# Kernel tuning notes

Measured on AMD Instinct MI355X. Metric: run time of the kernel, lower is better.

The kernel has to match this reference:

```python
import jax, jax.numpy as jnp
import numpy as np

N = 50000   # nodes per graph
E = 800000  # edges per graph (even, message() splits in half)
F = 100     # node/edge feature dim (init_count_size / init_emb_size)
D = 64      # hidden_dim3 = rule_graph_dim
W_SCALE = 0.05


def _mlp(x, w1, b1, w2, b2):
    return jax.nn.relu(x @ w1 + b1) @ w2 + b2


def _triple_conv(x, src, dst, ea, lw, lb, l2w, l2b, nn_fn):
    # PyG flow source_to_target: x_j = x[edge_index[0]], x_i = x[edge_index[1]]
    h = ea.shape[0] // 2
    x_j = x[src]
    x_i = x[dst]
    m1 = jax.nn.relu(jnp.concatenate([x_i[:h], ea[:h], x_j[:h]], 1) @ lw + lb)
    m2 = jax.nn.relu(jnp.concatenate([x_j[h:], ea[h:], x_i[h:]], 1) @ l2w + l2b)
    msgs = jnp.concatenate([m1, m2], 0)
    agg = jax.ops.segment_sum(msgs, dst, num_segments=x.shape[0])
    # eps = 0.0 buffer -> out = agg + (1+eps)*x = agg + x
    return nn_fn(agg + x)


def setup_inputs() -> dict:
    key = jax.random.key(0)
    ks = jax.random.split(key, 32)
    inp = {
        'features_1': jax.random.normal(ks[0], (N, F), jnp.float32),
        'edge_index_1': jax.random.randint(ks[1], (2, E), 0, N, jnp.int64 if jax.config.jax_enable_x64 else jnp.int32).astype(jnp.int32),
        'edge_attr_1': jax.random.normal(ks[2], (E, F), jnp.float32),
        'features_2': jax.random.normal(ks[3], (N, F), jnp.float32),
        'edge_index_2': jax.random.randint(ks[4], (2, E), 0, N, jnp.int32),
        'edge_attr_2': jax.random.normal(ks[5], (E, F), jnp.float32),
        'c1_lin_w': jax.random.normal(ks[6], (3 * F, F), jnp.float32) * W_SCALE,
        'c1_lin_b': jax.random.normal(ks[7], (F,), jnp.float32) * W_SCALE,
        'c1_lin2_w': jax.random.normal(ks[8], (3 * F, F), jnp.float32) * W_SCALE,
        'c1_lin2_b': jax.random.normal(ks[9], (F,), jnp.float32) * W_SCALE,
        'mlp1_w1': jax.random.normal(ks[10], (F, F), jnp.float32) * W_SCALE,
        'mlp1_b1': jax.random.normal(ks[11], (F,), jnp.float32) * W_SCALE,
        'mlp1_w2': jax.random.normal(ks[12], (F, F), jnp.float32) * W_SCALE,
        'mlp1_b2': jax.random.normal(ks[13], (F,), jnp.float32) * W_SCALE,
        'c2_lin_w': jax.random.normal(ks[14], (3 * F, F), jnp.float32) * W_SCALE,
        'c2_lin_b': jax.random.normal(ks[15], (F,), jnp.float32) * W_SCALE,
        'c2_lin2_w': jax.random.normal(ks[16], (3 * F, F), jnp.float32) * W_SCALE,
        'c2_lin2_b': jax.random.normal(ks[17], (F,), jnp.float32) * W_SCALE,
        'mlp2_w1': jax.random.normal(ks[18], (F, D), jnp.float32) * W_SCALE,
        'mlp2_b1': jax.random.normal(ks[19], (D,), jnp.float32) * W_SCALE,
        'mlp2_w2': jax.random.normal(ks[20], (D, D), jnp.float32) * W_SCALE,
        'mlp2_b2': jax.random.normal(ks[21], (D,), jnp.float32) * W_SCALE,
    }
    return inp


def reference(features_1, edge_index_1, edge_attr_1,
              features_2, edge_index_2, edge_attr_2,
              c1_lin_w, c1_lin_b, c1_lin2_w, c1_lin2_b,
              mlp1_w1, mlp1_b1, mlp1_w2, mlp1_b2,
              c2_lin_w, c2_lin_b, c2_lin2_w, c2_lin2_b,
              mlp2_w1, mlp2_b1, mlp2_w2, mlp2_b2):

    def conv_pass(x, ei, ea):
        src, dst = ei[0], ei[1]
        x = _triple_conv(x, src, dst, ea, c1_lin_w, c1_lin_b, c1_lin2_w, c1_lin2_b,
                         lambda z: _mlp(z, mlp1_w1, mlp1_b1, mlp1_w2, mlp1_b2))
        x = jax.nn.relu(x)
        x = _triple_conv(x, src, dst, ea, c2_lin_w, c2_lin_b, c2_lin2_w, c2_lin2_b,
                         lambda z: _mlp(z, mlp2_w1, mlp2_b1, mlp2_w2, mlp2_b2))
        return x

    f1 = conv_pass(features_1, edge_index_1, edge_attr_1)  # [N, D]
    f2 = conv_pass(features_2, edge_index_2, edge_attr_2)  # [N, D]
    # global_add_pool with a single batch id -> sum over nodes
    g1 = jnp.sum(f1, axis=0)
    g2 = jnp.sum(f2, axis=0)
    return jnp.stack([g1, g2], 0)  # [2, D]
```

## Files before the change

kernel.cpp:

```cpp
#include <hip/hip_runtime.h>

#define F 100
#define TS 256

typedef __attribute__((ext_vector_type(4))) unsigned short us4;
typedef __attribute__((ext_vector_type(8))) short short8;
typedef __attribute__((ext_vector_type(4))) float f32x4;

static __device__ __forceinline__ unsigned short f2bf(float f) {
    unsigned int u = __float_as_uint(f);
    unsigned int r = (u + 0x7FFF + ((u >> 16) & 1)) >> 16;
    return (unsigned short)r;
}
static __device__ __forceinline__ float bf2f(unsigned short u) {
    return __uint_as_float(((unsigned int)u) << 16);
}

__global__ __launch_bounds__(TS)
void hist2_kernel(const int* __restrict__ dst0, const int* __restrict__ dst1,
                  int h, int E, int N,
                  int* __restrict__ cnt1, int* __restrict__ cnt2)
{
    for (int idx = blockIdx.x * TS + threadIdx.x; idx < 2 * E; idx += gridDim.x * TS) {
        int g = idx >= E;
        int e = idx - g * E;
        int d = (g ? dst1 : dst0)[e];
        atomicAdd((e < h ? cnt1 : cnt2) + g * N + d, 1);
    }
}

__global__ __launch_bounds__(1024)
void scan4_kernel(const int* __restrict__ cnt1, const int* __restrict__ cnt2,
                  int* __restrict__ rp1, int* __restrict__ rp2, int n)
{
    const int which = blockIdx.x;
    const int hf = which >> 1, g = which & 1;
    const int* cnt = (hf ? cnt2 : cnt1) + g * n;
    int* rp = (hf ? rp2 : rp1) + g * (n + 1);
    __shared__ int buf[1024];
    __shared__ int carry_s;
    const int t = threadIdx.x;
    if (t == 0) carry_s = 0;
    __syncthreads();
    for (int base = 0; base < n; base += 8192) {
        int v[8], s = 0;
        #pragma unroll
        for (int j = 0; j < 8; ++j) {
            int idx = base + t * 8 + j;
            int x = (idx < n) ? cnt[idx] : 0;
            v[j] = s; s += x;
        }
        buf[t] = s;
        __syncthreads();
        for (int off = 1; off < 1024; off <<= 1) {
            int y = (t >= off) ? buf[t - off] : 0;
            __syncthreads();
            buf[t] += y;
            __syncthreads();
        }
        int excl = carry_s + buf[t] - s;
        #pragma unroll
        for (int j = 0; j < 8; ++j) {
            int idx = base + t * 8 + j;
            if (idx < n) rp[idx] = excl + v[j];
        }
        __syncthreads();
        if (t == 1023) carry_s += buf[1023];
        __syncthreads();
    }
    if (t == 0) rp[n] = carry_s;
}

__global__ __launch_bounds__(TS)
void scatter2_kernel(const int* __restrict__ src0, const int* __restrict__ dst0,
                     const int* __restrict__ src1, const int* __restrict__ dst1,
                     int h, int E, int N,
                     const int* __restrict__ rp1, const int* __restrict__ rp2,
                     int* __restrict__ cur1, int* __restrict__ cur2,
                     int* __restrict__ perm1, int* __restrict__ perm2,
                     int* __restrict__ es1, int* __restrict__ es2)
{
    for (int idx = blockIdx.x * TS + threadIdx.x; idx < 2 * E; idx += gridDim.x * TS) {
        int g = idx >= E;
        int e = idx - g * E;
        int d = (g ? dst1 : dst0)[e];
        int s = (g ? src1 : src0)[e];
        if (e < h) {
            int p = rp1[g * (N + 1) + d] + atomicAdd(&cur1[g * N + d], 1);
            perm1[g * h + p] = e; es1[g * h + p] = s + g * N;
        } else {
            int p = rp2[g * (N + 1) + d] + atomicAdd(&cur2[g * N + d], 1);
            perm2[g * h + p] = e; es2[g * h + p] = s + g * N;
        }
    }
}

__global__ __launch_bounds__(TS)
void pack_w_kernel(const float* w0, const float* w1, const float* w2, const float* w3,
                   unsigned short* __restrict__ Wp)
{
    int i = blockIdx.x * TS + threadIdx.x;
    if (i >= 12 * 112 * 128) return;
    int s = i / (112 * 128);
    int r = i - s * (112 * 128);
    int c = r >> 7, k = r & 127;
    int wi = s & 3, grp = s >> 2;
    const float* w = (wi == 0) ? w0 : (wi == 1) ? w1 : (wi == 2) ? w2 : w3;
    int off = (grp == 0) ? F : ((grp == 1) ? 0 : 2 * F);
    unsigned short v = 0;
    if (c < 100 && k < 100) v = f2bf(w[(off + k) * F + c]);
    Wp[i] = v;
}

__global__ __launch_bounds__(TS)
void pack_w2_kernel(const float* __restrict__ w, int K, int Nc, int ldb,
                    unsigned short* __restrict__ out)
{
    int i = blockIdx.x * TS + threadIdx.x;
    if (i >= 112 * 128) return;
    int c = i >> 7, k = i & 127;
    unsigned short v = 0;
    if (c < Nc && k < K) v = f2bf(w[k * ldb + c]);
    out[i] = v;
}

__global__ __launch_bounds__(TS)
void pack_x2_kernel(const float* __restrict__ x0, const float* __restrict__ x1,
                    int N, unsigned short* __restrict__ xb)
{
    const size_t total = (size_t)N * 2 * 32;
    for (size_t i = (size_t)blockIdx.x * TS + threadIdx.x; i < total; i += (size_t)gridDim.x * TS) {
        int n = (int)(i >> 5), q = (int)(i & 31);
        int g = n >= N;
        const float* x = g ? x1 : x0;
        int nl = n - g * N;
        us4 o = (us4){0, 0, 0, 0};
        if (q < 25) {
            float4 v = *(const float4*)&x[(size_t)nl * 100 + q * 4];
            o.x = f2bf(v.x); o.y = f2bf(v.y); o.z = f2bf(v.z); o.w = f2bf(v.w);
        }
        *(us4*)&xb[((size_t)n << 7) + q * 4] = o;
    }
}

__global__ __launch_bounds__(TS)
void gemm_node_mfma(const unsigned short* __restrict__ xb,
                    const unsigned short* __restrict__ B0, const unsigned short* __restrict__ B1,
                    const unsigned short* __restrict__ B2, const unsigned short* __restrict__ B3,
                    unsigned short* __restrict__ NTb,
                    int M)
{
    const int t = threadIdx.x, lane = t & 63, wv = t >> 6;
    const int rA = lane & 15, kg = lane >> 4;
    const unsigned short* Bp[4] = {B0, B1, B2, B3};
    const int ntiles = (M + 15) >> 4;
    for (int tile = blockIdx.x * 4 + wv; tile < ntiles; tile += gridDim.x * 4) {
        const int base = tile << 4;
        const int arow = min(base + rA, M - 1);
        short8 A[4];
        #pragma unroll
        for (int ks = 0; ks < 4; ++ks)
            A[ks] = *(const short8*)&xb[((size_t)arow << 7) + ks * 32 + kg * 8];
        const int row = base + rA;
        #pragma unroll
        for (int sel = 0; sel < 4; ++sel) {
            const unsigned short* B = Bp[sel];
            f32x4 C[7];
            #pragma unroll
            for (int nf = 0; nf < 7; ++nf) C[nf] = (f32x4){0.f, 0.f, 0.f, 0.f};
            #pragma unroll
            for (int ks = 0; ks < 4; ++ks) {
                #pragma unroll
                for (int nf = 0; nf < 7; ++nf) {
                    short8 Bf = *(const short8*)&B[(size_t)(rA + nf * 16) * 128 + ks * 32 + kg * 8];
                    C[nf] = __builtin_amdgcn_mfma_f32_16x16x32_bf16(Bf, A[ks], C[nf], 0, 0, 0);
                }
            }
            if (row < M) {
                #pragma unroll
                for (int nf = 0; nf < 7; ++nf) {
                    const int cb = nf * 16 + kg * 4;
                    if (cb < 100) {
                        us4 o;
                        o.x = f2bf(C[nf][0]); o.y = f2bf(C[nf][1]);
                        o.z = f2bf(C[nf][2]); o.w = f2bf(C[nf][3]);
                        *(us4*)&NTb[(size_t)row * 400 + sel * 100 + cb] = o;
                    }
                }
            }
        }
    }
}

__global__ __launch_bounds__(TS)
void gemm_edge_quad(const float* __restrict__ ea0, const float* __restrict__ ea1,
                    const int* __restrict__ perm,
                    const unsigned short* __restrict__ W0,
                    const unsigned short* __restrict__ W1,
                    unsigned short* __restrict__ P0,
                    unsigned short* __restrict__ P1,
                    int h)
{
    __shared__ unsigned short sA[2][64][136];
    const int t = threadIdx.x, lane = t & 63, wv = t >> 6;
    const int rA = lane & 15, kg = lane >> 4;
    const int M = 2 * h;
    const int ngrp = M >> 6;
    const int r_loc = t >> 2, sub = t & 3;

    int grp = blockIdx.x;
    if (grp >= ngrp) return;

    {
        const int grow = (grp << 6) + r_loc;
        const int g = grow >= h;
        const int e = perm[grow];
        const float* ea = (g ? ea1 : ea0) + (size_t)e * 100;
        float4 raw[7];
        #pragma unroll
        for (int j = 0; j < 7; ++j) {
            const int q = sub + 4 * j;
            if (q < 25) raw[j] = *(const float4*)&ea[q * 4];
        }
        #pragma unroll
        for (int j = 0; j < 8; ++j) {
            const int q = sub + 4 * j;
            us4 o = (us4){0, 0, 0, 0};
            if (j < 7 && q < 25) {
                o.x = f2bf(raw[j].x); o.y = f2bf(raw[j].y);
                o.z = f2bf(raw[j].z); o.w = f2bf(raw[j].w);
            }
            if (q < 32) *(us4*)&sA[0][r_loc][q * 4] = o;
        }
    }
    __syncthreads();

    int cur = 0;
    while (true) {
        const int nxt = grp + gridDim.x;
        const bool more = nxt < ngrp;

        float4 raw[7];
        if (more) {
            const int grow = (nxt << 6) + r_loc;
            const int g = grow >= h;
            const int e = perm[grow];
            const float* ea = (g ? ea1 : ea0) + (size_t)e * 100;
            #pragma unroll
            for (int j = 0; j < 7; ++j) {
                const int q = sub + 4 * j;
                if (q < 25) raw[j] = *(const float4*)&ea[q * 4];
            }
        }

        {
            const int lrow = wv * 16 + rA;
            short8 A[4];
            #pragma unroll
            for (int ks = 0; ks < 4; ++ks)
                A[ks] = *(const short8*)&sA[cur][lrow][ks * 32 + kg * 8];

            f32x4 C0[7], C1[7];
            #pragma unroll
            for (int nf = 0; nf < 7; ++nf) {
                C0[nf] = (f32x4){0.f, 0.f, 0.f, 0.f};
                C1[nf] = (f32x4){0.f, 0.f, 0.f, 0.f};
            }
            #pragma unroll
            for (int ks = 0; ks < 4; ++ks) {
                #pragma unroll
                for (int nf = 0; nf < 7; ++nf) {
                    short8 B0f = *(const short8*)&W0[(size_t)(rA + nf * 16) * 128 + ks * 32 + kg * 8];
                    C0[nf] = __builtin_amdgcn_mfma_f32_16x16x32_bf16(B0f, A[ks], C0[nf], 0, 0, 0);
                    short8 B1f = *(const short8*)&W1[(size_t)(rA + nf * 16) * 128 + ks * 32 + kg * 8];
                    C1[nf] = __builtin_amdgcn_mfma_f32_16x16x32_bf16(B1f, A[ks], C1[nf], 0, 0, 0);
                }
            }
            const int row = (grp << 6) + lrow;
            #pragma unroll
            for (int nf = 0; nf < 7; ++nf) {
                const int cb = nf * 16 + kg * 4;
                if (cb < 100) {
                    us4 o0, o1;
                    o0.x = f2bf(C0[nf][0]); o0.y = f2bf(C0[nf][1]);
                    o0.z = f2bf(C0[nf][2]); o0.w = f2bf(C0[nf][3]);
                    o1.x = f2bf(C1[nf][0]); o1.y = f2bf(C1[nf][1]);
                    o1.z = f2bf(C1[nf][2]); o1.w = f2bf(C1[nf][3]);
                    *(us4*)&P0[(size_t)row * 100 + cb] = o0;
                    *(us4*)&P1[(size_t)row * 100 + cb] = o1;
                }
            }
        }

        if (!more) break;

        #pragma unroll
        for (int j = 0; j < 8; ++j) {
            const int q = sub + 4 * j;
            us4 o = (us4){0, 0, 0, 0};
            if (j < 7 && q < 25) {
                o.x = f2bf(raw[j].x); o.y = f2bf(raw[j].y);
                o.z = f2bf(raw[j].z); o.w = f2bf(raw[j].w);
            }
            if (q < 32) *(us4*)&sA[cur ^ 1][r_loc][q * 4] = o;
        }
        __syncthreads();
        cur ^= 1; grp = nxt;
    }
}

__global__ __launch_bounds__(TS)
void seg_reduce_fused(const unsigned short* __restrict__ PA,
                      const unsigned short* __restrict__ PB,
                      const int* __restrict__ es1, const int* __restrict__ es2,
                      const int* __restrict__ rp1, const int* __restrict__ rp2,
                      const float* __restrict__ cb, const float* __restrict__ cb2,
                      const unsigned short* __restrict__ NTb,
                      const float* __restrict__ x0, const float* __restrict__ x1,
                      const unsigned short* __restrict__ xbin,
                      unsigned short* __restrict__ Ab,
                      int N, int h, int mode)
{
    const int gid = blockIdx.x * TS + threadIdx.x;
    const int n = gid >> 5, q = gid & 31;
    if (n >= 2 * N) return;
    const int c4 = q * 4;
    if (q >= 25) {
        *(us4*)&Ab[((size_t)n << 7) + c4] = (us4){0, 0, 0, 0};
        return;
    }
    const int g = n >= N;
    const int nl = n - g * N;

    float d1x, d1y, d1z, d1w, d2x, d2y, d2z, d2w;
    {
        const us4 vd1 = *(const us4*)&NTb[(size_t)n * 400 + 0 * 100 + c4];
        const float4 b1 = *(const float4*)&cb[c4];
        d1x = bf2f(vd1.x) + b1.x; d1y = bf2f(vd1.y) + b1.y;
        d1z = bf2f(vd1.z) + b1.z; d1w = bf2f(vd1.w) + b1.w;
        const us4 vd2 = *(const us4*)&NTb[(size_t)n * 400 + 3 * 100 + c4];
        const float4 b2 = *(const float4*)&cb2[c4];
        d2x = bf2f(vd2.x) + b2.x; d2y = bf2f(vd2.y) + b2.y;
        d2z = bf2f(vd2.z) + b2.z; d2w = bf2f(vd2.w) + b2.w;
    }
    const int* rpg1 = rp1 + g * (N + 1);
    const int* rpg2 = rp2 + g * (N + 1);
    int pos1 = max(rpg1[nl], 0) + g * h;
    const int end1 = min(rpg1[nl + 1], h) + g * h;
    int pos2 = max(rpg2[nl], 0) + g * h;
    const int end2 = min(rpg2[nl + 1], h) + g * h;

    float ax = 0.f, ay = 0.f, az = 0.f, aw = 0.f;

    const int common = min(end1 - pos1, end2 - pos2);
    #pragma unroll 2
    for (int i = 0; i < common; ++i) {
        const int s1 = es1[pos1 + i];
        const int s2 = es2[pos2 + i];
        const us4 pv1 = *(const us4*)&PA[(size_t)(pos1 + i) * 100 + c4];
        const us4 pv2 = *(const us4*)&PB[(size_t)(pos2 + i) * 100 + c4];
        const us4 v1 = *(const us4*)&NTb[(size_t)s1 * 400 + 1 * 100 + c4];
        const us4 v2 = *(const us4*)&NTb[(size_t)s2 * 400 + 2 * 100 + c4];
        ax += fmaxf(bf2f(pv1.x) + bf2f(v1.x) + d1x, 0.f)
            + fmaxf(bf2f(pv2.x) + bf2f(v2.x) + d2x, 0.f);
        ay += fmaxf(bf2f(pv1.y) + bf2f(v1.y) + d1y, 0.f)
            + fmaxf(bf2f(pv2.y) + bf2f(v2.y) + d2y, 0.f);
        az += fmaxf(bf2f(pv1.z) + bf2f(v1.z) + d1z, 0.f)
            + fmaxf(bf2f(pv2.z) + bf2f(v2.z) + d2z, 0.f);
        aw += fmaxf(bf2f(pv1.w) + bf2f(v1.w) + d1w, 0.f)
            + fmaxf(bf2f(pv2.w) + bf2f(v2.w) + d2w, 0.f);
    }
    pos1 += common; pos2 += common;

    #pragma unroll 2
    for (; pos1 < end1; ++pos1) {
        const int s = es1[pos1];
        const us4 pv = *(const us4*)&PA[(size_t)pos1 * 100 + c4];
        const us4 vs = *(const us4*)&NTb[(size_t)s * 400 + 1 * 100 + c4];
        ax += fmaxf(bf2f(pv.x) + bf2f(vs.x) + d1x, 0.f);
        ay += fmaxf(bf2f(pv.y) + bf2f(vs.y) + d1y, 0.f);
        az += fmaxf(bf2f(pv.z) + bf2f(vs.z) + d1z, 0.f);
        aw += fmaxf(bf2f(pv.w) + bf2f(vs.w) + d1w, 0.f);
    }
    #pragma unroll 2
    for (; pos2 < end2; ++pos2) {
        const int s = es2[pos2];
        const us4 pv = *(const us4*)&PB[(size_t)pos2 * 100 + c4];
        const us4 vs = *(const us4*)&NTb[(size_t)s * 400 + 2 * 100 + c4];
        ax += fmaxf(bf2f(pv.x) + bf2f(vs.x) + d2x, 0.f);
        ay += fmaxf(bf2f(pv.y) + bf2f(vs.y) + d2y, 0.f);
        az += fmaxf(bf2f(pv.z) + bf2f(vs.z) + d2z, 0.f);
        aw += fmaxf(bf2f(pv.w) + bf2f(vs.w) + d2w, 0.f);
    }

    float4 xv;
    if (mode == 0) {
        const float* x = g ? x1 : x0;
        xv = *(const float4*)&x[(size_t)nl * 100 + c4];
    } else {
        const us4 v = *(const us4*)&xbin[((size_t)n << 7) + c4];
        xv.x = bf2f(v.x); xv.y = bf2f(v.y); xv.z = bf2f(v.z); xv.w = bf2f(v.w);
    }
    us4 o;
    o.x = f2bf(ax + xv.x); o.y = f2bf(ay + xv.y);
    o.z = f2bf(az + xv.z); o.w = f2bf(aw + xv.w);
    *(us4*)&Ab[((size_t)n << 7) + c4] = o;
}

__global__ __launch_bounds__(TS)
void gemm_mlp_bf16out(const unsigned short* __restrict__ Ab,
                      const unsigned short* __restrict__ Wp,
                      const float* __restrict__ bias,
                      unsigned short* __restrict__ out,
                      int M, int Nc)
{
    const int t = threadIdx.x, lane = t & 63, wv = t >> 6;
    const int rA = lane & 15, kg = lane >> 4;
    const int ntiles = (M + 15) >> 4;
    for (int tile = blockIdx.x * 4 + wv; tile < ntiles; tile += gridDim.x * 4) {
        const int base = tile << 4;
        const int arow = min(base + rA, M - 1);
        f32x4 C[7];
        #pragma unroll
        for (int nf = 0; nf < 7; ++nf) C[nf] = (f32x4){0.f, 0.f, 0.f, 0.f};
        #pragma unroll
        for (int ks = 0; ks < 4; ++ks) {
            short8 A = *(const short8*)&Ab[((size_t)arow << 7) + ks * 32 + kg * 8];
            #pragma unroll
            for (int nf = 0; nf < 7; ++nf) {
                short8 B = *(const short8*)&Wp[(size_t)(rA + nf * 16) * 128 + ks * 32 + kg * 8];
                C[nf] = __builtin_amdgcn_mfma_f32_16x16x32_bf16(B, A, C[nf], 0, 0, 0);
            }
        }
        const int row = base + rA;
        if (row < M) {
            #pragma unroll
            for (int nf = 0; nf < 7; ++nf) {
                const int cb = nf * 16 + kg * 4;
                us4 o = (us4){0, 0, 0, 0};
                if (cb < Nc) {
                    float4 bv = *(const float4*)&bias[cb];
                    o.x = f2bf(fmaxf(C[nf][0] + bv.x, 0.f));
                    o.y = f2bf(fmaxf(C[nf][1] + bv.y, 0.f));
                    o.z = f2bf(fmaxf(C[nf][2] + bv.z, 0.f));
                    o.w = f2bf(fmaxf(C[nf][3] + bv.w, 0.f));
                }
                *(us4*)&out[((size_t)row << 7) + cb] = o;
            }
            *(us4*)&out[((size_t)row << 7) + 112 + kg * 4] = (us4){0, 0, 0, 0};
        }
    }
}

__global__ __launch_bounds__(TS)
void gemm_mlp_f32out(const unsigned short* __restrict__ Ab,
                     const unsigned short* __restrict__ Wp,
                     const float* __restrict__ bias,
                     float* __restrict__ out,
                     int M)
{
    const int t = threadIdx.x, lane = t & 63, wv = t >> 6;
    const int rA = lane & 15, kg = lane >> 4;
    const int ntiles = (M + 15) >> 4;
    for (int tile = blockIdx.x * 4 + wv; tile < ntiles; tile += gridDim.x * 4) {
        const int base = tile << 4;
        const int arow = min(base + rA, M - 1);
        f32x4 C[4];
        #pragma unroll
        for (int nf = 0; nf < 4; ++nf) C[nf] = (f32x4){0.f, 0.f, 0.f, 0.f};
        #pragma unroll
        for (int ks = 0; ks < 2; ++ks) {
            short8 A = *(const short8*)&Ab[((size_t)arow << 7) + ks * 32 + kg * 8];
            #pragma unroll
            for (int nf = 0; nf < 4; ++nf) {
                short8 B = *(const short8*)&Wp[(size_t)(rA + nf * 16) * 128 + ks * 32 + kg * 8];
                C[nf] = __builtin_amdgcn_mfma_f32_16x16x32_bf16(B, A, C[nf], 0, 0, 0);
            }
        }
        const int row = base + rA;
        if (row < M) {
            #pragma unroll
            for (int nf = 0; nf < 4; ++nf) {
                const int cb = nf * 16 + kg * 4;
                float4 bv = *(const float4*)&bias[cb];
                float4 o;
                o.x = C[nf][0] + bv.x; o.y = C[nf][1] + bv.y;
                o.z = C[nf][2] + bv.z; o.w = C[nf][3] + bv.w;
                *(float4*)&out[(size_t)row * 64 + cb] = o;
            }
        }
    }
}

__global__ __launch_bounds__(TS)
void colsum2_kernel(const float* __restrict__ Fm, int N, float* __restrict__ out)
{
    __shared__ float red[4][2][64];
    const int t = threadIdx.x;
    const int c = t & 63, rg = t >> 6;
    float s0 = 0.f, s1 = 0.f;
    const int M = 2 * N;
    for (int r = blockIdx.x * 4 + rg; r < M; r += gridDim.x * 4) {
        float v = Fm[(size_t)r * 64 + c];
        if (r < N) s0 += v; else s1 += v;
    }
    red[rg][0][c] = s0; red[rg][1][c] = s1;
    __syncthreads();
    if (rg == 0) {
        atomicAdd(&out[c],      red[0][0][c] + red[1][0][c] + red[2][0][c] + red[3][0][c]);
        atomicAdd(&out[64 + c], red[0][1][c] + red[1][1][c] + red[2][1][c] + red[3][1][c]);
    }
}

extern "C" void kernel_launch(void* const* d_in, const int* in_sizes, int n_in,
                              void* d_out, int out_size, void* d_ws, size_t ws_size,
                              hipStream_t stream)
{
    const int N = in_sizes[0] / F;
    const int E = in_sizes[1] / 2;
    const int h = E / 2;
    const int N2 = 2 * N, h2 = 2 * h;

    unsigned short* NTb  = (unsigned short*)d_ws;
    unsigned short* P1A = NTb + (size_t)N2 * 400;
    unsigned short* P1B = P1A + (size_t)h2 * 100;
    unsigned short* P2A = P1B + (size_t)h2 * 100;
    unsigned short* P2B = P2A + (size_t)h2 * 100;
    unsigned short* xb  = P2B + (size_t)h2 * 100;
    unsigned short* X1b = xb + (size_t)N2 * 128;
    unsigned short* Ab  = X1b + (size_t)N2 * 128;
    unsigned short* Hb  = Ab + (size_t)N2 * 128;
    float* F2  = (float*)(Hb + (size_t)N2 * 128);
    int* rp1   = (int*)(F2 + (size_t)N2 * 64);
    int* rp2   = rp1 + 2 * (N + 1);
    int* cnt1  = rp2 + 2 * (N + 1);
    int* cnt2  = cnt1 + N2;
    int* perm1 = cnt2 + N2;
    int* perm2 = perm1 + h2;
    int* es1   = perm2 + h2;
    int* es2   = es1 + h2;
    unsigned short* Wp = (unsigned short*)(es2 + h2);
    unsigned short* Wm = Wp + (size_t)12 * 112 * 128;

    const float* x0g0 = (const float*)d_in[0];
    const int*   ei0  = (const int*)d_in[1];
    const float* ea0  = (const float*)d_in[2];
    const float* x0g1 = (const float*)d_in[3];
    const int*   ei1  = (const int*)d_in[4];
    const float* ea1  = (const float*)d_in[5];
    const float* c1w  = (const float*)d_in[6];
    const float* c1b  = (const float*)d_in[7];
    const float* c1w2 = (const float*)d_in[8];
    const float* c1b2 = (const float*)d_in[9];
    const float* m1w1 = (const float*)d_in[10];
    const float* m1b1 = (const float*)d_in[11];
    const float* m1w2 = (const float*)d_in[12];
    const float* m1b2 = (const float*)d_in[13];
    const float* c2w  = (const float*)d_in[14];
    const float* c2b  = (const float*)d_in[15];
    const float* c2w2 = (const float*)d_in[16];
    const float* c2b2 = (const float*)d_in[17];
    const float* m2w1 = (const float*)d_in[18];
    const float* m2b1 = (const float*)d_in[19];
    const float* m2w2 = (const float*)d_in[20];
    const float* m2b2 = (const float*)d_in[21];

    hipMemsetAsync(d_out, 0, (size_t)out_size * sizeof(float), stream);

    const dim3 blk(TS);
    const size_t SL = (size_t)112 * 128;
    pack_w_kernel<<<(12 * 112 * 128 + TS - 1) / TS, blk, 0, stream>>>(c1w, c1w2, c2w, c2w2, Wp);
    pack_w2_kernel<<<56, blk, 0, stream>>>(m1w1, 100, 100, 100, Wm + 0 * SL);
    pack_w2_kernel<<<56, blk, 0, stream>>>(m1w2, 100, 100, 100, Wm + 1 * SL);
    pack_w2_kernel<<<56, blk, 0, stream>>>(m2w1, 100,  64,  64, Wm + 2 * SL);
    pack_w2_kernel<<<56, blk, 0, stream>>>(m2w2,  64,  64,  64, Wm + 3 * SL);

    hipMemsetAsync(cnt1, 0, 2 * (size_t)N2 * sizeof(int), stream);
    hist2_kernel<<<2048, blk, 0, stream>>>(ei0 + E, ei1 + E, h, E, N, cnt1, cnt2);
    scan4_kernel<<<4, 1024, 0, stream>>>(cnt1, cnt2, rp1, rp2, N);
    hipMemsetAsync(cnt1, 0, 2 * (size_t)N2 * sizeof(int), stream);
    scatter2_kernel<<<2048, blk, 0, stream>>>(ei0, ei0 + E, ei1, ei1 + E, h, E, N,
                                              rp1, rp2, cnt1, cnt2, perm1, perm2, es1, es2);
    pack_x2_kernel<<<2048, blk, 0, stream>>>(x0g0, x0g1, N, xb);

    gemm_edge_quad<<<2048, blk, 0, stream>>>(ea0, ea1, perm1,
                                             Wp + 0 * SL, Wp + 2 * SL, P1A, P2A, h);
    gemm_edge_quad<<<2048, blk, 0, stream>>>(ea0, ea1, perm2,
                                             Wp + 1 * SL, Wp + 3 * SL, P1B, P2B, h);

    const int nblkR = (N2 * 32 + TS - 1) / TS;
    for (int conv = 0; conv < 2; ++conv) {
        const float* cb  = conv ? c2b  : c1b;
        const float* cb2 = conv ? c2b2 : c1b2;
        const unsigned short* xin = conv ? X1b : xb;
        const int iw  = conv ? 2 : 0;
        const int iw2 = conv ? 3 : 1;
        const unsigned short* PA = conv ? P2A : P1A;
        const unsigned short* PB = conv ? P2B : P1B;

        gemm_node_mfma<<<2048, blk, 0, stream>>>(xin,
            Wp + (size_t)(4 + iw)  * SL, Wp + (size_t)(8 + iw)  * SL,
            Wp + (size_t)(4 + iw2) * SL, Wp + (size_t)(8 + iw2) * SL,
            NTb, N2);

        seg_reduce_fused<<<nblkR, blk, 0, stream>>>(PA, PB, es1, es2, rp1, rp2,
                                                    cb, cb2, NTb,
                                                    x0g0, x0g1, X1b, Ab,
                                                    N, h, conv);

        if (conv == 0) {
            gemm_mlp_bf16out<<<2048, blk, 0, stream>>>(Ab, Wm + 0 * SL, m1b1, Hb,  N2, 100);
            gemm_mlp_bf16out<<<2048, blk, 0, stream>>>(Hb, Wm + 1 * SL, m1b2, X1b, N2, 100);
        } else {
            gemm_mlp_bf16out<<<2048, blk, 0, stream>>>(Ab, Wm + 2 * SL, m2b1, Hb, N2, 64);
            gemm_mlp_f32out<<<2048, blk, 0, stream>>>(Hb, Wm + 3 * SL, m2b2, F2, N2);
        }
    }
    colsum2_kernel<<<512, blk, 0, stream>>>(F2, N, (float*)d_out);
    (void)ws_size; (void)n_in;
}
```

Baseline: 1.381 ms.

## Split edge GEMM weight pair across 8 waves with 512-thread blocks

The edge GEMM kernel now runs 512-thread blocks where waves 0-3 compute against the first weight matrix and waves 4-7 against the second, instead of each wave doing both. This halves per-wave accumulator registers and doubles the threads loading each 64-row tile of edge attributes, so each thread issues fewer global loads. A sched_barrier is placed after the prefetch loads to keep them ahead of the MFMA block. The cost is larger blocks that need more waves resident per CU for the same occupancy, plus each A fragment is now read from LDS by two waves.

```diff
diff --git a/kernel.cpp b/kernel.cpp
--- a/kernel.cpp
+++ b/kernel.cpp
@@ -192,7 +192,7 @@
     }
 }
 
-__global__ __launch_bounds__(TS)
+__global__ __launch_bounds__(512, 4)
 void gemm_edge_quad(const float* __restrict__ ea0, const float* __restrict__ ea1,
                     const int* __restrict__ perm,
                     const unsigned short* __restrict__ W0,
@@ -204,9 +204,12 @@
     __shared__ unsigned short sA[2][64][136];
     const int t = threadIdx.x, lane = t & 63, wv = t >> 6;
     const int rA = lane & 15, kg = lane >> 4;
+    const int lrow = (wv & 3) * 16 + rA;
+    const unsigned short* W = (wv >> 2) ? W1 : W0;
+    unsigned short* P = (wv >> 2) ? P1 : P0;
     const int M = 2 * h;
     const int ngrp = M >> 6;
-    const int r_loc = t >> 2, sub = t & 3;
+    const int r_loc = t >> 3, sub = t & 7;
 
     int grp = blockIdx.x;
     if (grp >= ngrp) return;
@@ -216,21 +219,21 @@
         const int g = grow >= h;
         const int e = perm[grow];
         const float* ea = (g ? ea1 : ea0) + (size_t)e * 100;
-        float4 raw[7];
-        #pragma unroll
-        for (int j = 0; j < 7; ++j) {
-            const int q = sub + 4 * j;
+        float4 raw[4];
+        #pragma unroll
+        for (int j = 0; j < 4; ++j) {
+            const int q = sub + 8 * j;
             if (q < 25) raw[j] = *(const float4*)&ea[q * 4];
         }
         #pragma unroll
-        for (int j = 0; j < 8; ++j) {
-            const int q = sub + 4 * j;
+        for (int j = 0; j < 4; ++j) {
+            const int q = sub + 8 * j;
             us4 o = (us4){0, 0, 0, 0};
-            if (j < 7 && q < 25) {
+            if (q < 25) {
                 o.x = f2bf(raw[j].x); o.y = f2bf(raw[j].y);
                 o.z = f2bf(raw[j].z); o.w = f2bf(raw[j].w);
             }
-            if (q < 32) *(us4*)&sA[0][r_loc][q * 4] = o;
+            *(us4*)&sA[0][r_loc][q * 4] = o;
         }
     }
     __syncthreads();
@@ -240,40 +243,35 @@
         const int nxt = grp + gridDim.x;
         const bool more = nxt < ngrp;
 
-        float4 raw[7];
+        float4 raw[4];
         if (more) {
             const int grow = (nxt << 6) + r_loc;
             const int g = grow >= h;
             const int e = perm[grow];
             const float* ea = (g ? ea1 : ea0) + (size_t)e * 100;
             #pragma unroll
-            for (int j = 0; j < 7; ++j) {
-                const int q = sub + 4 * j;
+            for (int j = 0; j < 4; ++j) {
+                const int q = sub + 8 * j;
                 if (q < 25) raw[j] = *(const float4*)&ea[q * 4];
             }
         }
+        __builtin_amdgcn_sched_barrier(0);
 
         {
-            const int lrow = wv * 16 + rA;
             short8 A[4];
             #pragma unroll
             for (int ks = 0; ks < 4; ++ks)
                 A[ks] = *(const short8*)&sA[cur][lrow][ks * 32 + kg * 8];
 
-            f32x4 C0[7], C1[7];
-            #pragma unroll
-            for (int nf = 0; nf < 7; ++nf) {
-                C0[nf] = (f32x4){0.f, 0.f, 0.f, 0.f};
-                C1[nf] = (f32x4){0.f, 0.f, 0.f, 0.f};
-            }
+            f32x4 C[7];
+            #pragma unroll
+            for (int nf = 0; nf < 7; ++nf) C[nf] = (f32x4){0.f, 0.f, 0.f, 0.f};
             #pragma unroll
             for (int ks = 0; ks < 4; ++ks) {
                 #pragma unroll
                 for (int nf = 0; nf < 7; ++nf) {
-                    short8 B0f = *(const short8*)&W0[(size_t)(rA + nf * 16) * 128 + ks * 32 + kg * 8];
-                    C0[nf] = __builtin_amdgcn_mfma_f32_16x16x32_bf16(B0f, A[ks], C0[nf], 0, 0, 0);
-                    short8 B1f = *(const short8*)&W1[(size_t)(rA + nf * 16) * 128 + ks * 32 + kg * 8];
-                    C1[nf] = __builtin_amdgcn_mfma_f32_16x16x32_bf16(B1f, A[ks], C1[nf], 0, 0, 0);
+                    short8 Bf = *(const short8*)&W[(size_t)(rA + nf * 16) * 128 + ks * 32 + kg * 8];
+                    C[nf] = __builtin_amdgcn_mfma_f32_16x16x32_bf16(Bf, A[ks], C[nf], 0, 0, 0);
                 }
             }
             const int row = (grp << 6) + lrow;
@@ -281,13 +279,10 @@
             for (int nf = 0; nf < 7; ++nf) {
                 const int cb = nf * 16 + kg * 4;
                 if (cb < 100) {
-                    us4 o0, o1;
-                    o0.x = f2bf(C0[nf][0]); o0.y = f2bf(C0[nf][1]);
-                    o0.z = f2bf(C0[nf][2]); o0.w = f2bf(C0[nf][3]);
-                    o1.x = f2bf(C1[nf][0]); o1.y = f2bf(C1[nf][1]);
-                    o1.z = f2bf(C1[nf][2]); o1.w = f2bf(C1[nf][3]);
-                    *(us4*)&P0[(size_t)row * 100 + cb] = o0;
-                    *(us4*)&P1[(size_t)row * 100 + cb] = o1;
+                    us4 o;
+                    o.x = f2bf(C[nf][0]); o.y = f2bf(C[nf][1]);
+                    o.z = f2bf(C[nf][2]); o.w = f2bf(C[nf][3]);
+                    *(us4*)&P[(size_t)row * 100 + cb] = o;
                 }
             }
         }
@@ -295,14 +290,14 @@
         if (!more) break;
 
         #pragma unroll
-        for (int j = 0; j < 8; ++j) {
-            const int q = sub + 4 * j;
+        for (int j = 0; j < 4; ++j) {
+            const int q = sub + 8 * j;
             us4 o = (us4){0, 0, 0, 0};
-            if (j < 7 && q < 25) {
+            if (q < 25) {
                 o.x = f2bf(raw[j].x); o.y = f2bf(raw[j].y);
                 o.z = f2bf(raw[j].z); o.w = f2bf(raw[j].w);
             }
-            if (q < 32) *(us4*)&sA[cur ^ 1][r_loc][q * 4] = o;
+            *(us4*)&sA[cur ^ 1][r_loc][q * 4] = o;
         }
         __syncthreads();
         cur ^= 1; grp = nxt;
@@ -583,10 +578,10 @@
                                               rp1, rp2, cnt1, cnt2, perm1, perm2, es1, es2);
     pack_x2_kernel<<<2048, blk, 0, stream>>>(x0g0, x0g1, N, xb);
 
-    gemm_edge_quad<<<2048, blk, 0, stream>>>(ea0, ea1, perm1,
-                                             Wp + 0 * SL, Wp + 2 * SL, P1A, P2A, h);
-    gemm_edge_quad<<<2048, blk, 0, stream>>>(ea0, ea1, perm2,
-                                             Wp + 1 * SL, Wp + 3 * SL, P1B, P2B, h);
+    gemm_edge_quad<<<2048, dim3(512), 0, stream>>>(ea0, ea1, perm1,
+                                                   Wp + 0 * SL, Wp + 2 * SL, P1A, P2A, h);
+    gemm_edge_quad<<<2048, dim3(512), 0, stream>>>(ea0, ea1, perm2,
+                                                   Wp + 1 * SL, Wp + 3 * SL, P1B, P2B, h);
 
     const int nblkR = (N2 * 32 + TS - 1) / TS;
     for (int conv = 0; conv < 2; ++conv) {
```

Result: slower. 1.786 ms (+29.3%).
